# Optimization experiments

Measured on AMD Instinct MI355X. Metric: run time of the kernel, lower is better.

The kernel has to match this reference:

```python
import jax, jax.numpy as jnp
import numpy as np

S = 3
K = 3
K2 = K * K
BN_EPS = 1e-5


def _conv(x, w, pad=0):
    return jax.lax.conv_general_dilated(
        x, w, window_strides=(1, 1), padding=[(pad, pad), (pad, pad)],
        dimension_numbers=('NCHW', 'OIHW', 'NCHW'))


def _adaptive_avg_pool(x, s):
    # PyTorch adaptive_avg_pool2d semantics: bin i covers [floor(i*H/s), ceil((i+1)*H/s))
    B, C, H, W = x.shape
    rows = []
    for i in range(s):
        h0, h1 = (i * H) // s, -(-((i + 1) * H) // s)
        cols = []
        for j in range(s):
            w0, w1 = (j * W) // s, -(-((j + 1) * W) // s)
            cols.append(x[:, :, h0:h1, w0:w1].mean(axis=(2, 3)))
        rows.append(jnp.stack(cols, axis=-1))
    return jnp.stack(rows, axis=-2)  # (B, C, s, s)


def _forward(c4, c5, w_to_fuse, bn_gamma, bn_beta, w_c4_proc, w_conv1,
             w_reshape, w_proj, w_sim4, w_sim5, kg_w1, kg_b1, kg_w2, kg_b2,
             mask_raw):
    B, C4, H, W = c4.shape
    H2, W2 = c5.shape[2], c5.shape[3]
    # nearest upsample c5 -> (H, W)
    ih = (jnp.arange(H) * H2) // H
    iw = (jnp.arange(W) * W2) // W
    c5_up = c5[:, :, ih][:, :, :, iw]

    c4_proc = _conv(c4, w_c4_proc, pad=1)
    c5_proc = _conv(c5_up, w_conv1)  # adaptive pool to (H,W) is identity here
    fused = c4_proc + c5_proc

    # to_fuse 1x1 conv -> BatchNorm (training-mode batch stats) -> SiLU
    y = _conv(fused, w_to_fuse)
    mu = y.mean(axis=(0, 2, 3), keepdims=True)
    var = y.var(axis=(0, 2, 3), keepdims=True)
    y = (y - mu) / jnp.sqrt(var + BN_EPS)
    X = jax.nn.silu(y * bn_gamma[None, :, None, None] + bn_beta[None, :, None, None])

    # patch descriptors and similarity (dot)
    p4 = _conv(_adaptive_avg_pool(c4, S), w_sim4)    # (B, sim, S, S)
    p5 = _conv(_adaptive_avg_pool(c5_up, S), w_sim5)
    sim = (p4 * p5).sum(axis=1)                      # (B, S, S)

    gated = sim.reshape(B, S * S) * jax.nn.sigmoid(mask_raw)[None, :]  # (B, S2)
    k_in = gated.reshape(B * S * S, 1)
    h = jax.nn.relu(k_in @ kg_w1.T + kg_b1)
    kernels = jax.nn.softmax((h @ kg_w2.T + kg_b2).reshape(B, S * S, K2), axis=-1)

    # unfold X: (B, C, K2, H, W) with torch row-major kernel-position order
    pad = K // 2
    Xp = jnp.pad(X, ((0, 0), (0, 0), (pad, pad), (pad, pad)))
    patches = jnp.stack([Xp[:, :, dy:dy + H, dx:dx + W]
                         for dy in range(K) for dx in range(K)], axis=2)

    # per-pixel patch index -> per-pixel kernel
    y_idx = jnp.clip((jnp.arange(H) * S) // H, 0, S - 1)
    x_idx = jnp.clip((jnp.arange(W) * S) // W, 0, S - 1)
    pidx = y_idx[:, None] * S + x_idx[None, :]       # (H, W) int
    kmap = kernels[:, pidx, :]                       # (B, H, W, K2)

    out = jnp.einsum('bckhw,bhwk->bchw', patches, kmap)

    fused_red = _conv(_conv(fused, w_reshape), w_proj)
    return out + fused_red


def setup_inputs() -> dict:
    key = jax.random.key(0)
    ks = jax.random.split(key, 16)
    B, C4, C5, H, W = 8, 256, 512, 64, 64
    OC, SIM, FR, HID = 256, 64, 128, 16
    n = jax.random.normal
    return {
        'c4': n(ks[0], (B, C4, H, W), dtype=jnp.float32),
        'c5': n(ks[1], (B, C5, H // 2, W // 2), dtype=jnp.float32),
        'w_to_fuse': n(ks[2], (OC, C4, 1, 1), dtype=jnp.float32) * 0.05,
        'bn_gamma': jnp.ones((OC,), dtype=jnp.float32),
        'bn_beta': jnp.zeros((OC,), dtype=jnp.float32),
        'w_c4_proc': n(ks[3], (C4, C4, 3, 3), dtype=jnp.float32) * 0.05,
        'w_conv1': n(ks[4], (C4, C5, 1, 1), dtype=jnp.float32) * 0.05,
        'w_reshape': n(ks[5], (FR, C4, 1, 1), dtype=jnp.float32) * 0.05,
        'w_proj': n(ks[6], (OC, FR, 1, 1), dtype=jnp.float32) * 0.05,
        'w_sim4': n(ks[7], (SIM, C4, 1, 1), dtype=jnp.float32) * 0.05,
        'w_sim5': n(ks[8], (SIM, C5, 1, 1), dtype=jnp.float32) * 0.05,
        'kg_w1': n(ks[9], (HID, 1), dtype=jnp.float32) * 0.5,
        'kg_b1': n(ks[10], (HID,), dtype=jnp.float32) * 0.1,
        'kg_w2': n(ks[11], (K2, HID), dtype=jnp.float32) * 0.5,
        'kg_b2': n(ks[12], (K2,), dtype=jnp.float32) * 0.1,
        'mask_raw': jnp.zeros((K2,), dtype=jnp.float32),
    }


def reference(c4, c5, w_to_fuse, bn_gamma, bn_beta, w_c4_proc, w_conv1,
              w_reshape, w_proj, w_sim4, w_sim5, kg_w1, kg_b1, kg_w2, kg_b2,
              mask_raw):
    return _forward(c4, c5, w_to_fuse, bn_gamma, bn_beta, w_c4_proc, w_conv1,
                    w_reshape, w_proj, w_sim4, w_sim5, kg_w1, kg_b1, kg_w2,
                    kg_b2, mask_raw)
```

## Files before the change

### kernel.cpp

```cpp
#include <hip/hip_runtime.h>
#include <cstddef>

#define B_   8
#define C4_  256
#define C5_  512
#define OC_  256
#define FR_  128
#define H_   64
#define W_   64
#define HW_  4096

typedef unsigned short u16;
typedef __bf16 bf16x8 __attribute__((ext_vector_type(8)));
typedef float floatx16 __attribute__((ext_vector_type(16)));

__device__ __forceinline__ u16 f2b(float x) {
    unsigned int u = __float_as_uint(x);
    return (u16)((u + 0x7FFFu + ((u >> 16) & 1u)) >> 16);
}
__device__ __forceinline__ float b2f(u16 x) {
    return __uint_as_float(((unsigned int)x) << 16);
}

__global__ __launch_bounds__(256) void pack_all(
    const float* __restrict__ w3, const float* __restrict__ w1,
    const float* __restrict__ wtf,
    const float* __restrict__ wp, const float* __restrict__ wr,
    const float* __restrict__ in4, const float* __restrict__ in5,
    u16* __restrict__ A3f, u16* __restrict__ A1f, u16* __restrict__ Wtff,
    u16* __restrict__ Wefff, u16* __restrict__ c4t, u16* __restrict__ c5f)
{
    __shared__ float sT[16448];
    const int t = threadIdx.x;
    const int blk = blockIdx.x;

    if (blk < 3072) {
        int i = blk * 256 + t;
        if (i < 589824) {
            int j  = i & 7;
            int l  = (i >> 3) & 63;
            int ks = (i >> 9) & 15;
            int ot = (i >> 13) & 7;
            int tap = i >> 16;
            int oc = ot * 32 + (l & 31);
            int c  = ks * 16 + ((l >> 5) << 3) + j;
            A3f[i] = f2b(w3[((size_t)oc * 256 + c) * 9 + tap]);
        } else if (i < 720896) {
            int i2 = i - 589824;
            int j  = i2 & 7;
            int l  = (i2 >> 3) & 63;
            int ks = (i2 >> 9) & 31;
            int ot = i2 >> 14;
            int oc = ot * 32 + (l & 31);
            int c  = ks * 16 + ((l >> 5) << 3) + j;
            A1f[i2] = f2b(w1[(size_t)oc * 512 + c]);
        } else {
            int i3 = i - 720896;
            int j  = i3 & 7;
            int l  = (i3 >> 3) & 63;
            int ks = (i3 >> 9) & 15;
            int ot = i3 >> 13;
            int oc = ot * 32 + (l & 31);
            int c  = ks * 16 + ((l >> 5) << 3) + j;
            Wtff[i3] = f2b(wtf[(size_t)oc * 256 + c]);
        }
    } else if (blk < 3328) {
        const int oc = blk - 3072, c = t;
        float s = 0.f;
        for (int f = 0; f < 128; ++f)
            s += wp[oc * 128 + f] * wr[f * 256 + c];
        int ot = oc >> 5;
        int lf = (oc & 31) + (((c >> 3) & 1) << 5);
        int ks = c >> 4;
        int j  = c & 7;
        Wefff[(((size_t)ot * 16 + ks) * 64 + lf) * 8 + j] = f2b(s);
    } else {
        const int id = blk - 3328;
        const int b = id / 96, x = id % 96;
        if (x < 64) {
            const int h = x;
            const int w = t & 63, cg = t >> 6;
            for (int i = 0; i < 64; ++i) {
                int c = cg * 64 + i;
                sT[w * 257 + c] = in4[(((size_t)b * 256 + c) * 64 + h) * 64 + w];
            }
            __syncthreads();
            for (int i = 0; i < 16; ++i) {
                int ww = cg * 16 + i;
                int c0 = (t & 63) * 4;
                ushort4 v;
                v.x = f2b(sT[ww * 257 + c0]);
                v.y = f2b(sT[ww * 257 + c0 + 1]);
                v.z = f2b(sT[ww * 257 + c0 + 2]);
                v.w = f2b(sT[ww * 257 + c0 + 3]);
                *(ushort4*)&c4t[(((size_t)b * 64 + h) * 64 + ww) * 256 + c0] = v;
            }
        } else {
            const int h2 = x - 64;
            const int w = t & 31, cg = t >> 5;
            for (int i = 0; i < 64; ++i) {
                int c = cg * 64 + i;
                sT[w * 513 + c] = in5[(((size_t)b * 512 + c) * 32 + h2) * 32 + w];
            }
            __syncthreads();
            u16* dstb = c5f + (size_t)(b * 32 + h2) * 32768;
            for (int i = 0; i < 32; ++i) {
                int id2 = i * 256 + t;
                int j0 = (id2 & 1) * 4;
                int l  = (id2 >> 1) & 63;
                int ks = (id2 >> 7) & 31;
                int n  = (id2 >> 12) & 1;
                int ch = ks * 16 + ((l >> 5) << 3) + j0;
                int w2 = (n * 32 + (l & 31)) >> 1;
                ushort4 v;
                v.x = f2b(sT[w2 * 513 + ch]);
                v.y = f2b(sT[w2 * 513 + ch + 1]);
                v.z = f2b(sT[w2 * 513 + ch + 2]);
                v.w = f2b(sT[w2 * 513 + ch + 3]);
                *(ushort4*)&dstb[id2 * 4] = v;
            }
        }
    }
}

__global__ __launch_bounds__(512, 1) void fuse_all(
    const u16* __restrict__ c4t, const u16* __restrict__ c5f,
    const u16* __restrict__ A3f, const u16* __restrict__ A1f,
    const u16* __restrict__ Wtff, const u16* __restrict__ Wefff,
    u16* __restrict__ yb, u16* __restrict__ outb, float* __restrict__ sums)
{
    extern __shared__ char smem[];
    float* lsum = (float*)(smem + 65536);
    float* lsq  = lsum + 256;

    const int t   = threadIdx.x;
    const int lin = blockIdx.x;
    const int d   = ((lin & 7) << 5) + (lin >> 3);
    const int b   = d >> 5;
    const int rp  = d & 31;
    const int h0  = rp * 2;

    const int l   = t & 63;
    const int w8  = t >> 6;
    const int og  = w8 >> 1;
    const int pg  = w8 & 1;
    const int lc  = l & 31;
    const int lg  = l >> 5;

    const int ocb = og * 64;
    const int otb = og * 2;

    if (t < 256) { lsum[t] = 0.f; lsq[t] = 0.f; }

    floatx16 acc[2][2];
    #pragma unroll
    for (int m = 0; m < 2; ++m)
        #pragma unroll
        for (int n = 0; n < 2; ++n)
            #pragma unroll
            for (int r = 0; r < 16; ++r)
                acc[m][n][r] = 0.f;

    for (int c0 = 0; c0 < 256; c0 += 64) {
        __syncthreads();
        for (int i = t; i < 2112; i += 512) {
            int px  = i >> 3, seg = i & 7;
            int gh  = h0 - 1 + px / 66;
            int gw  = (px % 66) - 1;
            int4 v = {0, 0, 0, 0};
            if (gh >= 0 && gh < 64 && gw >= 0 && gw < 64)
                v = *(const int4*)(c4t + ((((size_t)b * 64 + gh) * 64 + gw) << 8) + c0 + seg * 8);
            *(int4*)(smem + px * 128 + ((seg ^ (px & 7)) << 4)) = v;
        }
        __syncthreads();

        #pragma unroll
        for (int ky = 0; ky < 3; ++ky) {
            #pragma unroll
            for (int kx = 0; kx < 3; ++kx) {
                const int tap = ky * 3 + kx;
                #pragma unroll
                for (int kst = 0; kst < 4; ++kst) {
                    const int ksg = (c0 >> 4) + kst;
                    bf16x8 a[2], bb[2];
                    #pragma unroll
                    for (int m = 0; m < 2; ++m)
                        a[m] = *(const bf16x8*)(A3f + ((((size_t)tap * 8 + otb + m) * 16 + ksg) * 64 + l) * 8);
                    #pragma unroll
                    for (int n = 0; n < 2; ++n) {
                        const int pix = (pg + ky) * 66 + n * 32 + lc + kx;
                        const int seg = (kst * 2 + lg) ^ (pix & 7);
                        bb[n] = *(const bf16x8*)(smem + pix * 128 + (seg << 4));
                    }
                    #pragma unroll
                    for (int m = 0; m < 2; ++m)
                        #pragma unroll
                        for (int n = 0; n < 2; ++n)
                            acc[m][n] = __builtin_amdgcn_mfma_f32_32x32x16_bf16(
                                a[m], bb[n], acc[m][n], 0, 0, 0);
                }
            }
        }
    }

    const u16* c5b = c5f + (size_t)(b * 32 + rp) * 32768;
    #pragma unroll 4
    for (int ks = 0; ks < 32; ++ks) {
        bf16x8 a[2], bb[2];
        #pragma unroll
        for (int m = 0; m < 2; ++m)
            a[m] = *(const bf16x8*)(A1f + ((((size_t)otb + m) * 32 + ks) * 64 + l) * 8);
        #pragma unroll
        for (int n = 0; n < 2; ++n)
            bb[n] = *(const bf16x8*)(c5b + (((size_t)n * 32 + ks) * 64 + l) * 8);
        #pragma unroll
        for (int m = 0; m < 2; ++m)
            #pragma unroll
            for (int n = 0; n < 2; ++n)
                acc[m][n] = __builtin_amdgcn_mfma_f32_32x32x16_bf16(
                    a[m], bb[n], acc[m][n], 0, 0, 0);
    }

    __syncthreads();
    #pragma unroll
    for (int n = 0; n < 2; ++n) {
        const int px = pg * 64 + n * 32 + lc;
        #pragma unroll
        for (int m = 0; m < 2; ++m) {
            #pragma unroll
            for (int rq = 0; rq < 4; ++rq) {
                const int oc = ocb + m * 32 + rq * 8 + lg * 4;
                const int slot = oc >> 3;
                ushort4 v;
                v.x = f2b(acc[m][n][rq * 4 + 0]);
                v.y = f2b(acc[m][n][rq * 4 + 1]);
                v.z = f2b(acc[m][n][rq * 4 + 2]);
                v.w = f2b(acc[m][n][rq * 4 + 3]);
                *(ushort4*)(smem + px * 512 + ((slot ^ (px & 31)) << 4) + (oc & 7) * 2) = v;
            }
        }
    }
    __syncthreads();

    const bool isY = (w8 < 4);
    const u16* Wf  = isY ? Wtff : Wefff;
    u16* dst       = isY ? yb : outb;
    const int ot2  = (w8 & 3) * 2;

    #pragma unroll
    for (int ph = 0; ph < 2; ++ph) {
        floatx16 a2[2][2];
        #pragma unroll
        for (int m = 0; m < 2; ++m)
            #pragma unroll
            for (int n = 0; n < 2; ++n)
                #pragma unroll
                for (int r = 0; r < 16; ++r)
                    a2[m][n][r] = 0.f;

        #pragma unroll 4
        for (int ks = 0; ks < 16; ++ks) {
            bf16x8 a[2], bb[2];
            #pragma unroll
            for (int m = 0; m < 2; ++m)
                a[m] = *(const bf16x8*)(Wf + ((((size_t)ot2 + m) * 16 + ks) * 64 + l) * 8);
            #pragma unroll
            for (int n = 0; n < 2; ++n) {
                const int px = ph * 64 + n * 32 + lc;
                const int slot = ks * 2 + lg;
                bb[n] = *(const bf16x8*)(smem + px * 512 + ((slot ^ (px & 31)) << 4));
            }
            #pragma unroll
            for (int m = 0; m < 2; ++m)
                #pragma unroll
                for (int n = 0; n < 2; ++n)
                    a2[m][n] = __builtin_amdgcn_mfma_f32_32x32x16_bf16(
                        a[m], bb[n], a2[m][n], 0, 0, 0);
        }

        #pragma unroll
        for (int n = 0; n < 2; ++n) {
            const int px = ph * 64 + n * 32 + lc;
            const int row = px >> 6, wcol = px & 63;
            const size_t gp = (((size_t)b * 64 + h0 + row) * 64 + wcol) * 256;
            #pragma unroll
            for (int m = 0; m < 2; ++m) {
                #pragma unroll
                for (int rq = 0; rq < 4; ++rq) {
                    const int ocl = (w8 & 3) * 64 + m * 32 + rq * 8 + lg * 4;
                    ushort4 v;
                    v.x = f2b(a2[m][n][rq * 4 + 0]);
                    v.y = f2b(a2[m][n][rq * 4 + 1]);
                    v.z = f2b(a2[m][n][rq * 4 + 2]);
                    v.w = f2b(a2[m][n][rq * 4 + 3]);
                    *(ushort4*)&dst[gp + ocl] = v;
                }
            }
        }

        if (isY) {
            #pragma unroll
            for (int m = 0; m < 2; ++m) {
                #pragma unroll
                for (int r = 0; r < 16; ++r) {
                    float s = 0.f, q = 0.f;
                    #pragma unroll
                    for (int n = 0; n < 2; ++n) {
                        float v = a2[m][n][r];
                        s += v; q += v * v;
                    }
                    #pragma unroll
                    for (int off = 1; off < 32; off <<= 1) {
                        s += __shfl_xor(s, off);
                        q += __shfl_xor(q, off);
                    }
                    if (lc == 0) {
                        const int ocl = (w8 & 3) * 64 + m * 32 + (r & 3) + 8 * (r >> 2) + 4 * lg;
                        atomicAdd(&lsum[ocl], s);
                        atomicAdd(&lsq[ocl], q);
                    }
                }
            }
        }
    }

    __syncthreads();
    if (t < 256) {
        atomicAdd(&sums[t], lsum[t]);
        atomicAdd(&sums[256 + t], lsq[t]);
    }
}

__global__ __launch_bounds__(256) void pool_both(const float* __restrict__ in4,
                                                 const float* __restrict__ in5,
                                                 float* __restrict__ pool4,
                                                 float* __restrict__ pool5)
{
    __shared__ float colsum[4][64];
    const int i = blockIdx.x, b = blockIdx.z;
    const int t = threadIdx.x;
    const int ch = t >> 6, w = t & 63;
    const int h0 = (i * 64) / 3, h1 = ((i + 1) * 64 + 2) / 3;
    const bool is4 = (blockIdx.y < 64);
    const int cg = is4 ? blockIdx.y : (blockIdx.y - 64);
    const int c = cg * 4 + ch;

    float s = 0.f;
    for (int h = h0; h < h1; ++h) {
        float v = is4 ? in4[(((size_t)b * 256 + c) * 64 + h) * 64 + w]
                      : in5[(((size_t)b * 512 + c) * 32 + (h >> 1)) * 32 + (w >> 1)];
        s += v;
    }
    colsum[ch][w] = s;
    __syncthreads();
    if (t < 12) {
        int c2 = t / 3, j = t % 3;
        int w0 = (j * 64) / 3, w1 = ((j + 1) * 64 + 2) / 3;
        float tot = 0.f;
        for (int x = w0; x < w1; ++x) tot += colsum[c2][x];
        float r = tot / (float)((h1 - h0) * (w1 - w0));
        if (is4) pool4[(((size_t)b * 256 + cg * 4 + c2) * 3 + i) * 3 + j] = r;
        else     pool5[(((size_t)b * 512 + cg * 4 + c2) * 3 + i) * 3 + j] = r;
    }
}

__global__ __launch_bounds__(64) void sim_mlp(
    const float* __restrict__ pool4, const float* __restrict__ pool5,
    const float* __restrict__ w4, const float* __restrict__ w5,
    const float* __restrict__ kgw1, const float* __restrict__ kgb1,
    const float* __restrict__ kgw2, const float* __restrict__ kgb2,
    const float* __restrict__ mask, float* __restrict__ kers)
{
    const int r = blockIdx.x, b = blockIdx.y, m = threadIdx.x;
    float p4 = 0.f, p5 = 0.f;
    for (int c = 0; c < C4_; ++c)
        p4 += w4[(size_t)m * C4_ + c] * pool4[((size_t)b * C4_ + c) * 9 + r];
    for (int c = 0; c < C5_; ++c)
        p5 += w5[(size_t)m * C5_ + c] * pool5[((size_t)b * C5_ + c) * 9 + r];
    float v = p4 * p5;
    #pragma unroll
    for (int off = 32; off; off >>= 1) v += __shfl_down(v, off);
    if (m == 0) {
        float g = v * (1.f / (1.f + __expf(-mask[r])));
        float hb[16];
        #pragma unroll
        for (int j = 0; j < 16; ++j) hb[j] = fmaxf(g * kgw1[j] + kgb1[j], 0.f);
        float lg[9], mx = -1e30f;
        #pragma unroll
        for (int k = 0; k < 9; ++k) {
            float s = kgb2[k];
            #pragma unroll
            for (int j = 0; j < 16; ++j) s += kgw2[k * 16 + j] * hb[j];
            lg[k] = s;
            mx = fmaxf(mx, s);
        }
        float den = 0.f;
        #pragma unroll
        for (int k = 0; k < 9; ++k) { lg[k] = __expf(lg[k] - mx); den += lg[k]; }
        float inv = 1.f / den;
        #pragma unroll
        for (int k = 0; k < 9; ++k)
            kers[((size_t)b * 9 + r) * 9 + k] = lg[k] * inv;
    }
}

__global__ __launch_bounds__(256) void dynconv_bn(const u16* __restrict__ yb,
                                                  const u16* __restrict__ outb,
                                                  const float* __restrict__ sums,
                                                  const float* __restrict__ gamma,
                                                  const float* __restrict__ beta,
                                                  const float* __restrict__ kers,
                                                  float* __restrict__ out)
{
    __shared__ float sX[4][10][66];
    __shared__ float sK[81];
    __shared__ float sAB[8];
    const int t = threadIdx.x;
    const int r0 = blockIdx.x * 8, cg = blockIdx.y, b = blockIdx.z;
    const int ch = t >> 6, w = t & 63;
    const int c = cg * 4 + ch;

    if (t < 4) {
        const int cc = cg * 4 + t;
        const float n = (float)(B_ * HW_);
        float mu  = sums[cc] / n;
        float var = sums[256 + cc] / n - mu * mu;
        float a = gamma[cc] * rsqrtf(var + 1e-5f);
        sAB[t]     = a;
        sAB[4 + t] = beta[cc] - mu * a;
    }
    if (t < 81) sK[t] = kers[(size_t)b * 81 + t];
    __syncthreads();

    for (int idx = t; idx < 660; idx += 256) {
        int rr = idx / 66, cl = idx % 66;
        int gh = r0 - 1 + rr, gw = cl - 1;
        float v0 = 0.f, v1 = 0.f, v2 = 0.f, v3 = 0.f;
        if (gh >= 0 && gh < H_ && gw >= 0 && gw < W_) {
            ushort4 u = *(const ushort4*)&yb[((((size_t)b * 64 + gh) * 64 + gw) << 8) + cg * 4];
            float z;
            z = fmaf(sAB[0], b2f(u.x), sAB[4]); v0 = z / (1.f + __expf(-z));
            z = fmaf(sAB[1], b2f(u.y), sAB[5]); v1 = z / (1.f + __expf(-z));
            z = fmaf(sAB[2], b2f(u.z), sAB[6]); v2 = z / (1.f + __expf(-z));
            z = fmaf(sAB[3], b2f(u.w), sAB[7]); v3 = z / (1.f + __expf(-z));
        }
        sX[0][rr][cl] = v0;
        sX[1][rr][cl] = v1;
        sX[2][rr][cl] = v2;
        sX[3][rr][cl] = v3;
    }
    __syncthreads();

    const int rx = (w * 3) >> 6;
    for (int hh = 0; hh < 8; ++hh) {
        int h = r0 + hh;
        int ry = (h * 3) >> 6;
        const float* kp = &sK[(ry * 3 + rx) * 9];
        float acc = 0.f;
        #pragma unroll
        for (int dy = 0; dy < 3; ++dy)
            #pragma unroll
            for (int dx = 0; dx < 3; ++dx)
                acc += kp[dy * 3 + dx] * sX[ch][hh + dy][w + dx];
        acc += b2f(outb[((((size_t)b * 64 + h) * 64 + w) << 8) + c]);
        out[(((size_t)b * 256 + c) * H_ + h) * W_ + w] = acc;
    }
}

extern "C" void kernel_launch(void* const* d_in, const int* in_sizes, int n_in,
                              void* d_out, int out_size, void* d_ws, size_t ws_size,
                              hipStream_t stream)
{
    const float* c4       = (const float*)d_in[0];
    const float* c5       = (const float*)d_in[1];
    const float* w_to_fuse= (const float*)d_in[2];
    const float* bn_gamma = (const float*)d_in[3];
    const float* bn_beta  = (const float*)d_in[4];
    const float* w_c4_proc= (const float*)d_in[5];
    const float* w_conv1  = (const float*)d_in[6];
    const float* w_reshape= (const float*)d_in[7];
    const float* w_proj   = (const float*)d_in[8];
    const float* w_sim4   = (const float*)d_in[9];
    const float* w_sim5   = (const float*)d_in[10];
    const float* kg_w1    = (const float*)d_in[11];
    const float* kg_b1    = (const float*)d_in[12];
    const float* kg_w2    = (const float*)d_in[13];
    const float* kg_b2    = (const float*)d_in[14];
    const float* mask_raw = (const float*)d_in[15];

    float* out = (float*)d_out;

    u16*   yb    = (u16*)d_ws;
    u16*   outb  = yb + 8388608;
    u16*   c4t   = outb + 8388608;
    u16*   c5f   = c4t + 8388608;
    u16*   A3f   = c5f + 8388608;
    u16*   A1f   = A3f + 589824;
    u16*   Wtff  = A1f + 131072;
    u16*   Wefff = Wtff + 65536;
    float* pool4 = (float*)(Wefff + 65536);
    float* pool5 = pool4 + 18432;
    float* sums  = pool5 + 36864;
    float* kers  = sums + 512;

    hipMemsetAsync(sums, 0, 512 * sizeof(float), stream);

    pack_all<<<4096, 256, 0, stream>>>(w_c4_proc, w_conv1, w_to_fuse,
                                       w_proj, w_reshape, c4, c5,
                                       A3f, A1f, Wtff, Wefff, c4t, c5f);

    fuse_all<<<256, 512, 67584, stream>>>(c4t, c5f, A3f, A1f, Wtff, Wefff,
                                          yb, outb, sums);

    pool_both<<<dim3(3, 192, 8), 256, 0, stream>>>(c4, c5, pool4, pool5);

    sim_mlp<<<dim3(9, 8), 64, 0, stream>>>(pool4, pool5, w_sim4, w_sim5,
                                           kg_w1, kg_b1, kg_w2, kg_b2,
                                           mask_raw, kers);

    dynconv_bn<<<dim3(8, 64, 8), 256, 0, stream>>>(yb, outb, sums,
                                                   bn_gamma, bn_beta, kers, out);
}
```

Baseline: 232.5 us.

## Software-prefetch MFMA weight and c5 operands from global into registers

Restructures the 3x3 conv loop to iterate channel substeps outermost and holds all nine taps' weight fragments in registers, prefetching the next k-step's weights while the current MFMAs run. The 1x1 c5 GEMM and the second-stage projection GEMM get double-buffered register prefetch of their global operands. The aim is to hide global load latency behind MFMA work, at the cost of many more live VGPRs (18 bf16x8 fragments plus the accumulators), which can lower occupancy or cause spills.

```diff
diff --git a/kernel.cpp b/kernel.cpp
--- a/kernel.cpp
+++ b/kernel.cpp
@@ -161,6 +161,13 @@
             for (int r = 0; r < 16; ++r)
                 acc[m][n][r] = 0.f;
 
+    bf16x8 areg[9][2];
+    #pragma unroll
+    for (int tap = 0; tap < 9; ++tap)
+        #pragma unroll
+        for (int m = 0; m < 2; ++m)
+            areg[tap][m] = *(const bf16x8*)(A3f + ((((size_t)tap * 8 + otb + m) * 16 + 0) * 64 + l) * 8);
+
     for (int c0 = 0; c0 < 256; c0 += 64) {
         __syncthreads();
         for (int i = t; i < 2112; i += 512) {
@@ -174,18 +181,17 @@
         }
         __syncthreads();
 
-        #pragma unroll
-        for (int ky = 0; ky < 3; ++ky) {
-            #pragma unroll
-            for (int kx = 0; kx < 3; ++kx) {
-                const int tap = ky * 3 + kx;
-                #pragma unroll
-                for (int kst = 0; kst < 4; ++kst) {
-                    const int ksg = (c0 >> 4) + kst;
-                    bf16x8 a[2], bb[2];
-                    #pragma unroll
-                    for (int m = 0; m < 2; ++m)
-                        a[m] = *(const bf16x8*)(A3f + ((((size_t)tap * 8 + otb + m) * 16 + ksg) * 64 + l) * 8);
+        const int ksb = c0 >> 4;
+        #pragma unroll
+        for (int kst = 0; kst < 4; ++kst) {
+            const int ksgN = (kst < 3) ? (ksb + kst + 1)
+                                       : ((c0 < 192) ? ksb + 4 : 0);
+            #pragma unroll
+            for (int ky = 0; ky < 3; ++ky) {
+                #pragma unroll
+                for (int kx = 0; kx < 3; ++kx) {
+                    const int tap = ky * 3 + kx;
+                    bf16x8 bb[2];
                     #pragma unroll
                     for (int n = 0; n < 2; ++n) {
                         const int pix = (pg + ky) * 66 + n * 32 + lc + kx;
@@ -197,28 +203,40 @@
                         #pragma unroll
                         for (int n = 0; n < 2; ++n)
                             acc[m][n] = __builtin_amdgcn_mfma_f32_32x32x16_bf16(
-                                a[m], bb[n], acc[m][n], 0, 0, 0);
+                                areg[tap][m], bb[n], acc[m][n], 0, 0, 0);
+                    #pragma unroll
+                    for (int m = 0; m < 2; ++m)
+                        areg[tap][m] = *(const bf16x8*)(A3f + ((((size_t)tap * 8 + otb + m) * 16 + ksgN) * 64 + l) * 8);
                 }
             }
         }
     }
 
     const u16* c5b = c5f + (size_t)(b * 32 + rp) * 32768;
-    #pragma unroll 4
-    for (int ks = 0; ks < 32; ++ks) {
-        bf16x8 a[2], bb[2];
-        #pragma unroll
-        for (int m = 0; m < 2; ++m)
-            a[m] = *(const bf16x8*)(A1f + ((((size_t)otb + m) * 32 + ks) * 64 + l) * 8);
-        #pragma unroll
-        for (int n = 0; n < 2; ++n)
-            bb[n] = *(const bf16x8*)(c5b + (((size_t)n * 32 + ks) * 64 + l) * 8);
-        #pragma unroll
-        for (int m = 0; m < 2; ++m)
-            #pragma unroll
-            for (int n = 0; n < 2; ++n)
-                acc[m][n] = __builtin_amdgcn_mfma_f32_32x32x16_bf16(
-                    a[m], bb[n], acc[m][n], 0, 0, 0);
+    {
+        bf16x8 a1[2][2], b1[2][2];
+        #pragma unroll
+        for (int m = 0; m < 2; ++m) {
+            a1[0][m] = *(const bf16x8*)(A1f + ((((size_t)otb + m) * 32 + 0) * 64 + l) * 8);
+            b1[0][m] = *(const bf16x8*)(c5b + (((size_t)m * 32 + 0) * 64 + l) * 8);
+        }
+        #pragma unroll
+        for (int ks = 0; ks < 32; ++ks) {
+            const int cur = ks & 1, nxt = cur ^ 1;
+            if (ks < 31) {
+                #pragma unroll
+                for (int m = 0; m < 2; ++m) {
+                    a1[nxt][m] = *(const bf16x8*)(A1f + ((((size_t)otb + m) * 32 + ks + 1) * 64 + l) * 8);
+                    b1[nxt][m] = *(const bf16x8*)(c5b + (((size_t)m * 32 + ks + 1) * 64 + l) * 8);
+                }
+            }
+            #pragma unroll
+            for (int m = 0; m < 2; ++m)
+                #pragma unroll
+                for (int n = 0; n < 2; ++n)
+                    acc[m][n] = __builtin_amdgcn_mfma_f32_32x32x16_bf16(
+                        a1[cur][m], b1[cur][n], acc[m][n], 0, 0, 0);
+        }
     }
 
     __syncthreads();
@@ -258,12 +276,20 @@
                 for (int r = 0; r < 16; ++r)
                     a2[m][n][r] = 0.f;
 
-        #pragma unroll 4
+        bf16x8 wreg[2][2];
+        #pragma unroll
+        for (int m = 0; m < 2; ++m)
+            wreg[0][m] = *(const bf16x8*)(Wf + ((((size_t)ot2 + m) * 16 + 0) * 64 + l) * 8);
+
+        #pragma unroll
         for (int ks = 0; ks < 16; ++ks) {
-            bf16x8 a[2], bb[2];
-            #pragma unroll
-            for (int m = 0; m < 2; ++m)
-                a[m] = *(const bf16x8*)(Wf + ((((size_t)ot2 + m) * 16 + ks) * 64 + l) * 8);
+            const int cur = ks & 1, nxt = cur ^ 1;
+            if (ks < 15) {
+                #pragma unroll
+                for (int m = 0; m < 2; ++m)
+                    wreg[nxt][m] = *(const bf16x8*)(Wf + ((((size_t)ot2 + m) * 16 + ks + 1) * 64 + l) * 8);
+            }
+            bf16x8 bb[2];
             #pragma unroll
             for (int n = 0; n < 2; ++n) {
                 const int px = ph * 64 + n * 32 + lc;
@@ -275,7 +301,7 @@
                 #pragma unroll
                 for (int n = 0; n < 2; ++n)
                     a2[m][n] = __builtin_amdgcn_mfma_f32_32x32x16_bf16(
-                        a[m], bb[n], a2[m][n], 0, 0, 0);
+                        wreg[cur][m], bb[n], a2[m][n], 0, 0, 0);
         }
 
         #pragma unroll
```

After: 225.2 us. -3.2%, faster.
